# Kernel tuning notes

Measured on AMD Instinct MI355X. Metric: run time of the kernel, lower is better.

## Reference

```python
import jax, jax.numpy as jnp
import numpy as np

NEG_SLOPE = 0.01  # torch F.leaky_relu default used in the DGL GAT-style layer


def grat_layer(h, src, dst, W, a, n_nodes):
    """One GRAT (GAT-style) layer.
    h: [N, d_in], src/dst: [E] int, W: [d_in, d_out], a: [2*d_out] (attn_fc weight
    on concat [z_src || z_dst]). Returns [N, d_out].
    """
    d_out = W.shape[1]
    z = h @ W                                   # [N, d_out]
    # attention logits per edge: a^T [z_src || z_dst]
    s_src = z @ a[:d_out]                       # [N]
    s_dst = z @ a[d_out:]                       # [N]
    e = jax.nn.leaky_relu(s_src[src] + s_dst[dst], NEG_SLOPE)  # [E]
    # numerically stable softmax over incoming edges of each dst node
    m = jax.ops.segment_max(e, dst, num_segments=n_nodes)      # [N]
    m = jnp.where(jnp.isfinite(m), m, 0.0)      # nodes with no in-edges
    w = jnp.exp(e - m[dst])                     # [E]
    denom = jax.ops.segment_sum(w, dst, num_segments=n_nodes)  # [N]
    alpha = w / jnp.maximum(denom, 1e-9)[dst]   # [E]
    # weighted scatter-aggregate of source features into dst
    out = jax.ops.segment_sum(alpha[:, None] * z[src], dst, num_segments=n_nodes)
    return out                                  # [N, d_out]


def setup_inputs() -> dict:
    key = jax.random.key(0)
    ks = jax.random.split(key, 10)
    N, E = 100000, 1600000
    IN, H1, H2, OUT = 128, 32, 32, 1
    feature = jax.random.normal(ks[0], (N, IN), dtype=jnp.float32)
    src = jax.random.randint(ks[1], (E,), 0, N, dtype=jnp.int32)
    dst = jax.random.randint(ks[2], (E,), 0, N, dtype=jnp.int32)
    s = 0.1
    W1 = jax.random.normal(ks[3], (IN, H1), dtype=jnp.float32) * s
    a1 = jax.random.normal(ks[4], (2 * H1,), dtype=jnp.float32) * s
    W2 = jax.random.normal(ks[5], (H1, H2), dtype=jnp.float32) * s
    a2 = jax.random.normal(ks[6], (2 * H2,), dtype=jnp.float32) * s
    W3 = jax.random.normal(ks[7], (H2, OUT), dtype=jnp.float32) * s
    a3 = jax.random.normal(ks[8], (2 * OUT,), dtype=jnp.float32) * s
    return {"feature": feature, "src": src, "dst": dst,
            "W1": W1, "a1": a1, "W2": W2, "a2": a2, "W3": W3, "a3": a3}


def reference(feature, src, dst, W1, a1, W2, a2, W3, a3):
    n = feature.shape[0]
    h = jax.nn.relu(grat_layer(feature, src, dst, W1, a1, n))
    h = jax.nn.relu(grat_layer(h, src, dst, W2, a2, n))
    h = grat_layer(h, src, dst, W3, a3, n)
    return jax.nn.sigmoid(h)                    # [N, 1]
```

## Files before the change

kernel.cpp:

```cpp
#include <hip/hip_runtime.h>
#include <hip/hip_bf16.h>
#include <cstdint>
#include <cstddef>

#define NEG_SLOPE 0.01f

static __device__ __forceinline__ unsigned short f2bf(float f) {
    __hip_bfloat16 b = __float2bfloat16(f);
    return *(unsigned short*)&b;
}


__global__ __launch_bounds__(128) void gemm1_kernel(
    const float* __restrict__ h, const float* __restrict__ W,
    const float* __restrict__ a, unsigned short* __restrict__ zb,
    float* __restrict__ s_src, float* __restrict__ s_dst, int N)
{
    __shared__ float Wl[128 * 32];
    int tid = threadIdx.x;
    int rowBase = blockIdx.x * 64;

    {
        const float4* W4 = (const float4*)W;
        float4* Wl4 = (float4*)Wl;
        for (int i = tid; i < 1024; i += 128) Wl4[i] = W4[i];
    }
    __syncthreads();

    int wv   = tid >> 6;
    int lane = tid & 63;
    int g    = lane >> 3;
    int l8   = lane & 7;
    int r0   = wv * 32 + g * 4;
    int col4 = l8 * 4;

    float acc[4][4];
#pragma unroll
    for (int i = 0; i < 4; i++)
#pragma unroll
        for (int c = 0; c < 4; c++) acc[i][c] = 0.f;

    const float4* h4  = (const float4*)h;
    const float4* Wl4 = (const float4*)Wl;

    size_t rowOff[4];
#pragma unroll
    for (int i = 0; i < 4; i++) {
        int r = rowBase + r0 + i;
        rowOff[i] = (size_t)((r < N) ? r : (N - 1)) * 32;
    }

#pragma unroll 2
    for (int kq = 0; kq < 32; kq++) {
        float4 w0 = Wl4[(kq * 4 + 0) * 8 + l8];
        float4 w1 = Wl4[(kq * 4 + 1) * 8 + l8];
        float4 w2 = Wl4[(kq * 4 + 2) * 8 + l8];
        float4 w3 = Wl4[(kq * 4 + 3) * 8 + l8];
#pragma unroll
        for (int i = 0; i < 4; i++) {
            float4 hv = h4[rowOff[i] + kq];
            acc[i][0] += hv.x * w0.x; acc[i][1] += hv.x * w0.y;
            acc[i][2] += hv.x * w0.z; acc[i][3] += hv.x * w0.w;
            acc[i][0] += hv.y * w1.x; acc[i][1] += hv.y * w1.y;
            acc[i][2] += hv.y * w1.z; acc[i][3] += hv.y * w1.w;
            acc[i][0] += hv.z * w2.x; acc[i][1] += hv.z * w2.y;
            acc[i][2] += hv.z * w2.z; acc[i][3] += hv.z * w2.w;
            acc[i][0] += hv.w * w3.x; acc[i][1] += hv.w * w3.y;
            acc[i][2] += hv.w * w3.z; acc[i][3] += hv.w * w3.w;
        }
    }

    float4 alo = ((const float4*)a)[l8];
    float4 ahi = ((const float4*)a)[8 + l8];
#pragma unroll
    for (int i = 0; i < 4; i++) {
        int row = rowBase + r0 + i;
        if (row < N) {
            ushort4 zv4 = make_ushort4(f2bf(acc[i][0]), f2bf(acc[i][1]),
                                       f2bf(acc[i][2]), f2bf(acc[i][3]));
            *(ushort4*)&zb[(size_t)row * 32 + col4] = zv4;
            float ps = acc[i][0] * alo.x + acc[i][1] * alo.y + acc[i][2] * alo.z + acc[i][3] * alo.w;
            float pd = acc[i][0] * ahi.x + acc[i][1] * ahi.y + acc[i][2] * ahi.z + acc[i][3] * ahi.w;
            ps += __shfl_xor(ps, 1, 64); ps += __shfl_xor(ps, 2, 64); ps += __shfl_xor(ps, 4, 64);
            pd += __shfl_xor(pd, 1, 64); pd += __shfl_xor(pd, 2, 64); pd += __shfl_xor(pd, 4, 64);
            if (l8 == 0) { s_src[row] = ps; s_dst[row] = pd; }
        }
    }
}


#define TILE_E 4096
#define NB_MAX 512

__global__ __launch_bounds__(256) void csr_hist_kernel(
    const int* __restrict__ dst, int* __restrict__ counts,
    int E, int TB, int NB)
{
    __shared__ int hist[NB_MAX];
    int tid = threadIdx.x;
    int t = blockIdx.x;
    for (int b = tid; b < NB; b += 256) hist[b] = 0;
    __syncthreads();
    int base = t * TILE_E;
    for (int i = tid; i < TILE_E; i += 256) {
        int k = base + i;
        if (k < E) atomicAdd(&hist[dst[k] >> 8], 1);
    }
    __syncthreads();
    for (int b = tid; b < NB; b += 256) counts[b * TB + t] = hist[b];
}

__global__ __launch_bounds__(256) void scan1_kernel(
    const int* __restrict__ vals, int* __restrict__ incl,
    int* __restrict__ blockSums, int M)
{
    __shared__ int tmp[256];
    int tid = threadIdx.x;
    int i = blockIdx.x * 256 + tid;
    int v = (i < M) ? vals[i] : 0;
    tmp[tid] = v;
    __syncthreads();
#pragma unroll
    for (int off = 1; off < 256; off <<= 1) {
        int t = (tid >= off) ? tmp[tid - off] : 0;
        __syncthreads();
        tmp[tid] += t;
        __syncthreads();
    }
    if (i < M) incl[i] = tmp[tid];
    if (tid == 255) blockSums[blockIdx.x] = tmp[255];
}

__global__ __launch_bounds__(256) void scan3_kernel(
    const int* __restrict__ vals, const int* __restrict__ blockSums,
    int* __restrict__ cscan, int M, int E)
{
    __shared__ int red[256];
    int tid = threadIdx.x;
    int bid = blockIdx.x;
    int partial = 0;
    for (int j = tid; j < bid; j += 256) partial += blockSums[j];
    red[tid] = partial;
    __syncthreads();
#pragma unroll
    for (int off = 128; off > 0; off >>= 1) {
        if (tid < off) red[tid] += red[tid + off];
        __syncthreads();
    }
    int prefix = red[0];
    int i = bid * 256 + tid;
    if (i < M) cscan[i] = cscan[i] - vals[i] + prefix;
    if (i == 0) cscan[M] = E;
}

__global__ __launch_bounds__(256) void csr_scatter_kernel(
    const int* __restrict__ src, const int* __restrict__ dst,
    const int* __restrict__ cscan, int* __restrict__ ebuf,
    int E, int TB, int NB)
{
    __shared__ int baseB[NB_MAX];
    __shared__ int cur[NB_MAX];
    int tid = threadIdx.x;
    int t = blockIdx.x;
    for (int b = tid; b < NB; b += 256) {
        baseB[b] = cscan[b * TB + t];
        cur[b] = 0;
    }
    __syncthreads();
    int base = t * TILE_E;
    for (int i = tid; i < TILE_E; i += 256) {
        int k = base + i;
        if (k < E) {
            int d = dst[k], s = src[k];
            int b = d >> 8;
            int r = atomicAdd(&cur[b], 1);
            ebuf[baseB[b] + r] = (s << 8) | (d & 255);
        }
    }
}

__global__ __launch_bounds__(256) void csr_bucket_kernel(
    const int* __restrict__ ebuf, const int* __restrict__ cscan,
    int* __restrict__ csr_src, int* __restrict__ offsets,
    int N, int E, int TB)
{
    __shared__ int eb[8192];
    __shared__ int hist[256];
    __shared__ int loff[256];
    __shared__ int tmp[256];
    int tid = threadIdx.x;
    int b = blockIdx.x;

    int beg = cscan[b * TB];
    int endv = cscan[(b + 1) * TB];
    int cnt = endv - beg;
    int first = b << 8;

    hist[tid] = 0;
    __syncthreads();

    bool inLds = (cnt <= 8192);
    for (int i = tid; i < cnt; i += 256) {
        int v = ebuf[beg + i];
        if (inLds) eb[i] = v;
        atomicAdd(&hist[v & 255], 1);
    }
    __syncthreads();

    int hv = hist[tid];
    tmp[tid] = hv;
    __syncthreads();
#pragma unroll
    for (int off = 1; off < 256; off <<= 1) {
        int t = (tid >= off) ? tmp[tid - off] : 0;
        __syncthreads();
        tmp[tid] += t;
        __syncthreads();
    }
    loff[tid] = tmp[tid] - hv;
    __syncthreads();

    if (first + tid < N) offsets[first + tid] = beg + loff[tid];
    if (b == 0 && tid == 0) offsets[N] = E;

    hist[tid] = 0;
    __syncthreads();

    for (int i = tid; i < cnt; i += 256) {
        int v = inLds ? eb[i] : ebuf[beg + i];
        int d8 = v & 255;
        int r = atomicAdd(&hist[d8], 1);
        csr_src[beg + loff[d8] + r] = v >> 8;
    }
}


#define AGG32_PRELOAD(S_SRC, S_DST)                                           \
    int nodeC = (node < N) ? node : (N - 1);                                  \
    int beg = offsets[nodeC], end = offsets[nodeC + 1];                       \
    int deg = end - beg;                                                      \
    float sd = (S_DST)[nodeC];                                                \
    int pfx = beg + lane;                                                     \
    int s_pre = (deg <= 32 && pfx < end) ? csr_src[pfx] : 0;                  \
    float w_pre = 0.f;                                                        \
    if (deg <= 32 && pfx < end) {                                             \
        float e = (S_SRC)[s_pre] + sd;                                        \
        e = (e > 0.f) ? e : NEG_SLOPE * e;                                    \
        w_pre = __expf(e);                                                    \
    }

#define AGG32_CORE(S_SRC, S_DST, ZB)                                          \
    int q  = lane >> 3;                                                       \
    int c4 = (lane & 7) * 4;                                                  \
    unsigned cb = (unsigned)(lane & 7) * 8u;                                  \
    const char* zbc = (const char*)(ZB);                                      \
    float4 o4 = make_float4(0.f, 0.f, 0.f, 0.f);                              \
    float rden;                                                               \
    if (deg <= 32) {                                                          \
        int soff = s_pre << 6;                                                \
        int e0 = __shfl(soff, q + 0,  32);                                    \
        int e1 = __shfl(soff, q + 4,  32);                                    \
        int e2 = __shfl(soff, q + 8,  32);                                    \
        int e3 = __shfl(soff, q + 12, 32);                                    \
        uint2 g0 = *(const uint2*)(zbc + (cb + (unsigned)e0));                \
        uint2 g1 = *(const uint2*)(zbc + (cb + (unsigned)e1));                \
        uint2 g2 = *(const uint2*)(zbc + (cb + (unsigned)e2));                \
        uint2 g3 = *(const uint2*)(zbc + (cb + (unsigned)e3));                \
        int dgt = (deg > 16);                                                 \
        uint2 g4, g5, g6, g7;                                                 \
        if (dgt) {                                                            \
            int e4 = __shfl(soff, q + 16, 32);                                \
            int e5 = __shfl(soff, q + 20, 32);                                \
            int e6 = __shfl(soff, q + 24, 32);                                \
            int e7 = __shfl(soff, q + 28, 32);                                \
            g4 = *(const uint2*)(zbc + (cb + (unsigned)e4));                  \
            g5 = *(const uint2*)(zbc + (cb + (unsigned)e5));                  \
            g6 = *(const uint2*)(zbc + (cb + (unsigned)e6));                  \
            g7 = *(const uint2*)(zbc + (cb + (unsigned)e7));                  \
        }                                                                     \
        float l = w_pre;                                                      \
        _Pragma("unroll")                                                     \
        for (int off = 16; off > 0; off >>= 1) l += __shfl_xor(l, off, 32);   \
        rden = 1.f / fmaxf(l, 1e-9f);                                         \
        float w0 = __shfl(w_pre, q + 0,  32);                                 \
        float w1 = __shfl(w_pre, q + 4,  32);                                 \
        float w2 = __shfl(w_pre, q + 8,  32);                                 \
        float w3 = __shfl(w_pre, q + 12, 32);                                 \
        o4.x += w0 * __uint_as_float(g0.x << 16);                             \
        o4.y += w0 * __uint_as_float(g0.x & 0xffff0000u);                     \
        o4.z += w0 * __uint_as_float(g0.y << 16);                             \
        o4.w += w0 * __uint_as_float(g0.y & 0xffff0000u);                     \
        o4.x += w1 * __uint_as_float(g1.x << 16);                             \
        o4.y += w1 * __uint_as_float(g1.x & 0xffff0000u);                     \
        o4.z += w1 * __uint_as_float(g1.y << 16);                             \
        o4.w += w1 * __uint_as_float(g1.y & 0xffff0000u);                     \
        o4.x += w2 * __uint_as_float(g2.x << 16);                             \
        o4.y += w2 * __uint_as_float(g2.x & 0xffff0000u);                     \
        o4.z += w2 * __uint_as_float(g2.y << 16);                             \
        o4.w += w2 * __uint_as_float(g2.y & 0xffff0000u);                     \
        o4.x += w3 * __uint_as_float(g3.x << 16);                             \
        o4.y += w3 * __uint_as_float(g3.x & 0xffff0000u);                     \
        o4.z += w3 * __uint_as_float(g3.y << 16);                             \
        o4.w += w3 * __uint_as_float(g3.y & 0xffff0000u);                     \
        if (dgt) {                                                            \
            float w4 = __shfl(w_pre, q + 16, 32);                             \
            float w5 = __shfl(w_pre, q + 20, 32);                             \
            float w6 = __shfl(w_pre, q + 24, 32);                             \
            float w7 = __shfl(w_pre, q + 28, 32);                             \
            o4.x += w4 * __uint_as_float(g4.x << 16);                         \
            o4.y += w4 * __uint_as_float(g4.x & 0xffff0000u);                 \
            o4.z += w4 * __uint_as_float(g4.y << 16);                         \
            o4.w += w4 * __uint_as_float(g4.y & 0xffff0000u);                 \
            o4.x += w5 * __uint_as_float(g5.x << 16);                         \
            o4.y += w5 * __uint_as_float(g5.x & 0xffff0000u);                 \
            o4.z += w5 * __uint_as_float(g5.y << 16);                         \
            o4.w += w5 * __uint_as_float(g5.y & 0xffff0000u);                 \
            o4.x += w6 * __uint_as_float(g6.x << 16);                         \
            o4.y += w6 * __uint_as_float(g6.x & 0xffff0000u);                 \
            o4.z += w6 * __uint_as_float(g6.y << 16);                         \
            o4.w += w6 * __uint_as_float(g6.y & 0xffff0000u);                 \
            o4.x += w7 * __uint_as_float(g7.x << 16);                         \
            o4.y += w7 * __uint_as_float(g7.x & 0xffff0000u);                 \
            o4.z += w7 * __uint_as_float(g7.y << 16);                         \
            o4.w += w7 * __uint_as_float(g7.y & 0xffff0000u);                 \
        }                                                                     \
    } else {                                                                  \
        float l = 0.f;                                                        \
        for (int p = beg + lane; p < end; p += 32) {                          \
            float e = (S_SRC)[csr_src[p]] + sd;                               \
            e = (e > 0.f) ? e : NEG_SLOPE * e;                                \
            l += __expf(e);                                                   \
        }                                                                     \
        _Pragma("unroll")                                                     \
        for (int off = 16; off > 0; off >>= 1) l += __shfl_xor(l, off, 32);   \
        rden = 1.f / fmaxf(l, 1e-9f);                                         \
        for (int p = 0; p < deg; p += 4) {                                    \
            int idx = p + q;                                                  \
            int valid = (idx < deg);                                          \
            int s = csr_src[beg + (valid ? idx : deg - 1)];                   \
            float e = (S_SRC)[s] + sd;                                        \
            e = (e > 0.f) ? e : NEG_SLOPE * e;                                \
            float w = valid ? __expf(e) : 0.f;                                \
            uint2 u = *(const uint2*)(zbc + (cb + ((unsigned)s << 6)));       \
            o4.x += w * __uint_as_float(u.x << 16);                           \
            o4.y += w * __uint_as_float(u.x & 0xffff0000u);                   \
            o4.z += w * __uint_as_float(u.y << 16);                           \
            o4.w += w * __uint_as_float(u.y & 0xffff0000u);                   \
        }                                                                     \
    }                                                                         \
    o4.x += __shfl_xor(o4.x, 8, 32);                                          \
    o4.y += __shfl_xor(o4.y, 8, 32);                                          \
    o4.z += __shfl_xor(o4.z, 8, 32);                                          \
    o4.w += __shfl_xor(o4.w, 8, 32);                                          \
    o4.x += __shfl_xor(o4.x, 16, 32);                                         \
    o4.y += __shfl_xor(o4.y, 16, 32);                                         \
    o4.z += __shfl_xor(o4.z, 16, 32);                                         \
    o4.w += __shfl_xor(o4.w, 16, 32);                                         \
    float4 vv4;                                                               \
    vv4.x = fmaxf(o4.x * rden, 0.f);                                          \
    vv4.y = fmaxf(o4.y * rden, 0.f);                                          \
    vv4.z = fmaxf(o4.z * rden, 0.f);                                          \
    vv4.w = fmaxf(o4.w * rden, 0.f);

__global__ __launch_bounds__(256) void agg32_l1_kernel(
    const int* __restrict__ offsets, const int* __restrict__ csr_src,
    const float* __restrict__ s_src1, const float* __restrict__ s_dst1,
    const unsigned short* __restrict__ zb1,
    const float* __restrict__ W2, const float* __restrict__ a2,
    unsigned short* __restrict__ zb2,
    float* __restrict__ s_src2, float* __restrict__ s_dst2, int N)
{
    __shared__ float W2l[32 * 32];
    __shared__ float hl[8 * 32];
    int tid  = threadIdx.x;
    int g    = tid >> 5;
    int lane = tid & 31;
    int node = blockIdx.x * 8 + g;

    AGG32_PRELOAD(s_src1, s_dst1)

    for (int i = tid; i < 1024; i += 256) W2l[i] = W2[i];
    __syncthreads();

    if (node >= N) return;

    AGG32_CORE(s_src1, s_dst1, zb1)

    if (q == 0) *(float4*)&hl[g * 32 + c4] = vv4;
    const float4* hb4 = (const float4*)&hl[g * 32];
    float acc2 = 0.f;
#pragma unroll
    for (int c = 0; c < 8; ++c) {
        float4 hv = hb4[c];
        acc2 += hv.x * W2l[(c * 4 + 0) * 32 + lane];
        acc2 += hv.y * W2l[(c * 4 + 1) * 32 + lane];
        acc2 += hv.z * W2l[(c * 4 + 2) * 32 + lane];
        acc2 += hv.w * W2l[(c * 4 + 3) * 32 + lane];
    }

    zb2[(size_t)node * 32 + lane] = f2bf(acc2);
    float ps = acc2 * a2[lane];
    float pd = acc2 * a2[32 + lane];
#pragma unroll
    for (int off = 16; off > 0; off >>= 1) {
        ps += __shfl_xor(ps, off, 32);
        pd += __shfl_xor(pd, off, 32);
    }
    if (lane == 0) { s_src2[node] = ps; s_dst2[node] = pd; }
}

__global__ __launch_bounds__(256) void agg32_l2_kernel(
    const int* __restrict__ offsets, const int* __restrict__ csr_src,
    const float* __restrict__ s_src2, const float* __restrict__ s_dst2,
    const unsigned short* __restrict__ zb2,
    const float* __restrict__ W3, const float* __restrict__ a3,
    float* __restrict__ zs, float* __restrict__ s_dst3, int N)
{
    int tid  = threadIdx.x;
    int g    = tid >> 5;
    int lane = tid & 31;
    int node = blockIdx.x * 8 + g;
    if (node >= N) return;

    AGG32_PRELOAD(s_src2, s_dst2)
    AGG32_CORE(s_src2, s_dst2, zb2)

    float4 w3q = ((const float4*)W3)[lane & 7];
    float t = vv4.x * w3q.x + vv4.y * w3q.y + vv4.z * w3q.z + vv4.w * w3q.w;
    t += __shfl_xor(t, 1, 32);
    t += __shfl_xor(t, 2, 32);
    t += __shfl_xor(t, 4, 32);
    if (lane == 0) {
        zs[node] = t;
        s_dst3[node] = t * a3[1];
    }
}

__global__ __launch_bounds__(256) void agg1_fused_kernel(
    const int* __restrict__ offsets, const int* __restrict__ csr_src,
    const float* __restrict__ zs, const float* __restrict__ a3,
    const float* __restrict__ s_dst, float* __restrict__ out, int N)
{
    int node = blockIdx.x * 8 + (threadIdx.x >> 5);
    int lane = threadIdx.x & 31;
    if (node >= N) return;

    int beg = offsets[node], end = offsets[node + 1];
    float sd = s_dst[node];
    float a30 = a3[0];

    float l = 0.f, o = 0.f;
    for (int p = beg + lane; p < end; p += 32) {
        float z = zs[csr_src[p]];
        float e = z * a30 + sd;
        e = (e > 0.f) ? e : NEG_SLOPE * e;
        float w = __expf(e);
        l += w;
        o += w * z;
    }
#pragma unroll
    for (int off = 16; off > 0; off >>= 1) {
        l += __shfl_xor(l, off, 32);
        o += __shfl_xor(o, off, 32);
    }
    if (lane == 0) {
        float v = o / fmaxf(l, 1e-9f);
        out[node] = 1.f / (1.f + __expf(-v));
    }
}


extern "C" void kernel_launch(void* const* d_in, const int* in_sizes, int n_in,
                              void* d_out, int out_size, void* d_ws, size_t ws_size,
                              hipStream_t stream)
{
    const float* feature = (const float*)d_in[0];
    const int*   src     = (const int*)d_in[1];
    const int*   dst     = (const int*)d_in[2];
    const float* W1      = (const float*)d_in[3];
    const float* a1      = (const float*)d_in[4];
    const float* W2      = (const float*)d_in[5];
    const float* a2      = (const float*)d_in[6];
    const float* W3      = (const float*)d_in[7];
    const float* a3      = (const float*)d_in[8];
    float* out = (float*)d_out;

    const int N = in_sizes[0] / 128;
    const int E = in_sizes[1];

    const int TB = (E + TILE_E - 1) / TILE_E;
    const int NB = (N + 255) >> 8;
    const int M  = NB * TB;

    char* p = (char*)d_ws;
    unsigned short* zb1 = (unsigned short*)p;  p += (size_t)N * 32 * sizeof(unsigned short);
    unsigned short* zb2 = (unsigned short*)p;  p += (size_t)N * 32 * sizeof(unsigned short);
    float* zs32    = (float*)p;  p += (size_t)N * 2 * sizeof(float);
    float* s_src1  = (float*)p;  p += (size_t)N * sizeof(float);
    float* s_dst1  = (float*)p;  p += (size_t)N * sizeof(float);
    float* s_src2  = (float*)p;  p += (size_t)N * sizeof(float);
    float* s_dst2  = (float*)p;  p += (size_t)N * sizeof(float);
    float* s_dst3  = (float*)p;  p += (size_t)N * sizeof(float);
    int*   offsets = (int*)p;    p += ((size_t)N + 1) * sizeof(int);
    int*   counts  = (int*)p;    p += ((size_t)M + 1) * sizeof(int);
    int*   cscan   = (int*)p;    p += ((size_t)M + 1) * sizeof(int);
    int*   blockSums = (int*)p;  p += 1024 * sizeof(int);
    int*   ebuf    = (int*)p;    p += (size_t)E * sizeof(int);
    int*   csr_src = (int*)p;    p += (size_t)E * sizeof(int);

    const int nodeBlocks8  = (N + 7) / 8;
    const int gemmBlocks64 = (N + 63) / 64;
    const int scanBlocksM  = (M + 255) / 256;

    hipLaunchKernelGGL(csr_hist_kernel, dim3(TB), dim3(256), 0, stream,
                       dst, counts, E, TB, NB);
    hipLaunchKernelGGL(scan1_kernel, dim3(scanBlocksM), dim3(256), 0, stream,
                       counts, cscan, blockSums, M);
    hipLaunchKernelGGL(scan3_kernel, dim3(scanBlocksM), dim3(256), 0, stream,
                       counts, blockSums, cscan, M, E);
    hipLaunchKernelGGL(csr_scatter_kernel, dim3(TB), dim3(256), 0, stream,
                       src, dst, cscan, ebuf, E, TB, NB);
    hipLaunchKernelGGL(csr_bucket_kernel, dim3(NB), dim3(256), 0, stream,
                       ebuf, cscan, csr_src, offsets, N, E, TB);

    hipLaunchKernelGGL(gemm1_kernel, dim3(gemmBlocks64), dim3(128), 0, stream,
                       feature, W1, a1, zb1, s_src1, s_dst1, N);
    hipLaunchKernelGGL(agg32_l1_kernel, dim3(nodeBlocks8), dim3(256), 0, stream,
                       offsets, csr_src, s_src1, s_dst1, zb1, W2, a2,
                       zb2, s_src2, s_dst2, N);

    hipLaunchKernelGGL(agg32_l2_kernel, dim3(nodeBlocks8), dim3(256), 0, stream,
                       offsets, csr_src, s_src2, s_dst2, zb2, W3, a3,
                       zs32, s_dst3, N);

    hipLaunchKernelGGL(agg1_fused_kernel, dim3(nodeBlocks8), dim3(256), 0, stream,
                       offsets, csr_src, zs32, a3, s_dst3, out, N);
}
```

Measured before the change: 243.1 us.

## Replace two-level bucketed CSR build with per-node global atomic counting sort

Swaps the tiled LDS-histogram plus bucket-sort CSR construction for a direct global-atomic approach: zero per-node counts, count in-degrees with atomics, scan them into offsets, then scatter sources using an atomic cursor per node. This drops the intermediate edge buffer and the second bucketing pass. In exchange it performs 3.2M global atomics on scattered addresses, and the order of edges within each node's list becomes nondeterministic. That can change floating-point summation order and lowers locality in the scatter.

```diff
diff --git a/kernel.cpp b/kernel.cpp
--- a/kernel.cpp
+++ b/kernel.cpp
@@ -89,25 +89,18 @@
 }
 
 
-#define TILE_E 4096
-#define NB_MAX 512
-
-__global__ __launch_bounds__(256) void csr_hist_kernel(
-    const int* __restrict__ dst, int* __restrict__ counts,
-    int E, int TB, int NB)
-{
-    __shared__ int hist[NB_MAX];
-    int tid = threadIdx.x;
-    int t = blockIdx.x;
-    for (int b = tid; b < NB; b += 256) hist[b] = 0;
-    __syncthreads();
-    int base = t * TILE_E;
-    for (int i = tid; i < TILE_E; i += 256) {
-        int k = base + i;
-        if (k < E) atomicAdd(&hist[dst[k] >> 8], 1);
-    }
-    __syncthreads();
-    for (int b = tid; b < NB; b += 256) counts[b * TB + t] = hist[b];
+__global__ __launch_bounds__(256) void zero_kernel(int* __restrict__ p, int n)
+{
+    int stride = gridDim.x * 256;
+    for (int i = blockIdx.x * 256 + threadIdx.x; i < n; i += stride) p[i] = 0;
+}
+
+__global__ __launch_bounds__(256) void count_kernel(
+    const int* __restrict__ dst, int* __restrict__ counts, int E)
+{
+    int stride = gridDim.x * 256;
+    for (int i = blockIdx.x * 256 + threadIdx.x; i < E; i += stride)
+        atomicAdd(&counts[dst[i]], 1);
 }
 
 __global__ __launch_bounds__(256) void scan1_kernel(
@@ -131,9 +124,10 @@
     if (tid == 255) blockSums[blockIdx.x] = tmp[255];
 }
 
-__global__ __launch_bounds__(256) void scan3_kernel(
-    const int* __restrict__ vals, const int* __restrict__ blockSums,
-    int* __restrict__ cscan, int M, int E)
+__global__ __launch_bounds__(256) void scan_offsets_kernel(
+    const int* __restrict__ vals, const int* __restrict__ incl,
+    const int* __restrict__ blockSums,
+    int* __restrict__ offsets, int* __restrict__ cursor, int Nn, int E)
 {
     __shared__ int red[256];
     int tid = threadIdx.x;
@@ -149,88 +143,23 @@
     }
     int prefix = red[0];
     int i = bid * 256 + tid;
-    if (i < M) cscan[i] = cscan[i] - vals[i] + prefix;
-    if (i == 0) cscan[M] = E;
-}
-
-__global__ __launch_bounds__(256) void csr_scatter_kernel(
+    if (i < Nn) {
+        int v = incl[i] - vals[i] + prefix;
+        offsets[i] = v;
+        cursor[i]  = v;
+    }
+    if (i == 0) offsets[Nn] = E;
+}
+
+__global__ __launch_bounds__(256) void scatter_atomic_kernel(
     const int* __restrict__ src, const int* __restrict__ dst,
-    const int* __restrict__ cscan, int* __restrict__ ebuf,
-    int E, int TB, int NB)
-{
-    __shared__ int baseB[NB_MAX];
-    __shared__ int cur[NB_MAX];
-    int tid = threadIdx.x;
-    int t = blockIdx.x;
-    for (int b = tid; b < NB; b += 256) {
-        baseB[b] = cscan[b * TB + t];
-        cur[b] = 0;
-    }
-    __syncthreads();
-    int base = t * TILE_E;
-    for (int i = tid; i < TILE_E; i += 256) {
-        int k = base + i;
-        if (k < E) {
-            int d = dst[k], s = src[k];
-            int b = d >> 8;
-            int r = atomicAdd(&cur[b], 1);
-            ebuf[baseB[b] + r] = (s << 8) | (d & 255);
-        }
-    }
-}
-
-__global__ __launch_bounds__(256) void csr_bucket_kernel(
-    const int* __restrict__ ebuf, const int* __restrict__ cscan,
-    int* __restrict__ csr_src, int* __restrict__ offsets,
-    int N, int E, int TB)
-{
-    __shared__ int eb[8192];
-    __shared__ int hist[256];
-    __shared__ int loff[256];
-    __shared__ int tmp[256];
-    int tid = threadIdx.x;
-    int b = blockIdx.x;
-
-    int beg = cscan[b * TB];
-    int endv = cscan[(b + 1) * TB];
-    int cnt = endv - beg;
-    int first = b << 8;
-
-    hist[tid] = 0;
-    __syncthreads();
-
-    bool inLds = (cnt <= 8192);
-    for (int i = tid; i < cnt; i += 256) {
-        int v = ebuf[beg + i];
-        if (inLds) eb[i] = v;
-        atomicAdd(&hist[v & 255], 1);
-    }
-    __syncthreads();
-
-    int hv = hist[tid];
-    tmp[tid] = hv;
-    __syncthreads();
-#pragma unroll
-    for (int off = 1; off < 256; off <<= 1) {
-        int t = (tid >= off) ? tmp[tid - off] : 0;
-        __syncthreads();
-        tmp[tid] += t;
-        __syncthreads();
-    }
-    loff[tid] = tmp[tid] - hv;
-    __syncthreads();
-
-    if (first + tid < N) offsets[first + tid] = beg + loff[tid];
-    if (b == 0 && tid == 0) offsets[N] = E;
-
-    hist[tid] = 0;
-    __syncthreads();
-
-    for (int i = tid; i < cnt; i += 256) {
-        int v = inLds ? eb[i] : ebuf[beg + i];
-        int d8 = v & 255;
-        int r = atomicAdd(&hist[d8], 1);
-        csr_src[beg + loff[d8] + r] = v >> 8;
+    int* __restrict__ cursor, int* __restrict__ csr_src, int E)
+{
+    int stride = gridDim.x * 256;
+    for (int i = blockIdx.x * 256 + threadIdx.x; i < E; i += stride) {
+        int d = dst[i];
+        int pos = atomicAdd(&cursor[d], 1);
+        csr_src[pos] = src[i];
     }
 }
 
@@ -488,10 +417,6 @@
     const int N = in_sizes[0] / 128;
     const int E = in_sizes[1];
 
-    const int TB = (E + TILE_E - 1) / TILE_E;
-    const int NB = (N + 255) >> 8;
-    const int M  = NB * TB;
-
     char* p = (char*)d_ws;
     unsigned short* zb1 = (unsigned short*)p;  p += (size_t)N * 32 * sizeof(unsigned short);
     unsigned short* zb2 = (unsigned short*)p;  p += (size_t)N * 32 * sizeof(unsigned short);
@@ -502,26 +427,28 @@
     float* s_dst2  = (float*)p;  p += (size_t)N * sizeof(float);
     float* s_dst3  = (float*)p;  p += (size_t)N * sizeof(float);
     int*   offsets = (int*)p;    p += ((size_t)N + 1) * sizeof(int);
-    int*   counts  = (int*)p;    p += ((size_t)M + 1) * sizeof(int);
-    int*   cscan   = (int*)p;    p += ((size_t)M + 1) * sizeof(int);
+    int*   counts  = (int*)p;    p += ((size_t)N + 1) * sizeof(int);
+    int*   incl    = (int*)p;    p += ((size_t)N + 1) * sizeof(int);
+    int*   cursor  = (int*)p;    p += ((size_t)N + 1) * sizeof(int);
     int*   blockSums = (int*)p;  p += 1024 * sizeof(int);
-    int*   ebuf    = (int*)p;    p += (size_t)E * sizeof(int);
     int*   csr_src = (int*)p;    p += (size_t)E * sizeof(int);
 
     const int nodeBlocks8  = (N + 7) / 8;
     const int gemmBlocks64 = (N + 63) / 64;
-    const int scanBlocksM  = (M + 255) / 256;
-
-    hipLaunchKernelGGL(csr_hist_kernel, dim3(TB), dim3(256), 0, stream,
-                       dst, counts, E, TB, NB);
-    hipLaunchKernelGGL(scan1_kernel, dim3(scanBlocksM), dim3(256), 0, stream,
-                       counts, cscan, blockSums, M);
-    hipLaunchKernelGGL(scan3_kernel, dim3(scanBlocksM), dim3(256), 0, stream,
-                       counts, blockSums, cscan, M, E);
-    hipLaunchKernelGGL(csr_scatter_kernel, dim3(TB), dim3(256), 0, stream,
-                       src, dst, cscan, ebuf, E, TB, NB);
-    hipLaunchKernelGGL(csr_bucket_kernel, dim3(NB), dim3(256), 0, stream,
-                       ebuf, cscan, csr_src, offsets, N, E, TB);
+    const int scanBlocksN  = (N + 255) / 256;
+    int edgeBlocks = (E + 255) / 256;
+    if (edgeBlocks > 2048) edgeBlocks = 2048;
+
+    hipLaunchKernelGGL(zero_kernel, dim3(scanBlocksN), dim3(256), 0, stream,
+                       counts, N);
+    hipLaunchKernelGGL(count_kernel, dim3(edgeBlocks), dim3(256), 0, stream,
+                       dst, counts, E);
+    hipLaunchKernelGGL(scan1_kernel, dim3(scanBlocksN), dim3(256), 0, stream,
+                       counts, incl, blockSums, N);
+    hipLaunchKernelGGL(scan_offsets_kernel, dim3(scanBlocksN), dim3(256), 0, stream,
+                       counts, incl, blockSums, offsets, cursor, N, E);
+    hipLaunchKernelGGL(scatter_atomic_kernel, dim3(edgeBlocks), dim3(256), 0, stream,
+                       src, dst, cursor, csr_src, E);
 
     hipLaunchKernelGGL(gemm1_kernel, dim3(gemmBlocks64), dim3(128), 0, stream,
                        feature, W1, a1, zb1, s_src1, s_dst1, N);
```

New measurement: 400.1 us. +64.6%, slower.
